# Optimization experiments

Measured on AMD Instinct MI355X. Metric: run time of the kernel, lower is better.

## Reference

```python
import jax, jax.numpy as jnp
import numpy as np

RADIUS = 5
EPS = 1e-08


def _box_blur(x, r):
    """Normalized (2r+1)x(2r+1) box filter with reflect padding, NCHW."""
    k = 2 * r + 1
    B, C, H, W = x.shape
    xp = jnp.pad(x, ((0, 0), (0, 0), (r, r), (r, r)), mode='reflect')
    y = xp.reshape(B * C, 1, H + 2 * r, W + 2 * r)
    kh = jnp.ones((1, 1, k, 1), x.dtype) / k
    kw = jnp.ones((1, 1, 1, k), x.dtype) / k
    y = jax.lax.conv_general_dilated(y, kh, (1, 1), 'VALID')
    y = jax.lax.conv_general_dilated(y, kw, (1, 1), 'VALID')
    return y.reshape(B, C, H, W)


def setup_inputs() -> dict:
    key = jax.random.key(0)
    k1, k2 = jax.random.split(key)
    feat = jax.random.uniform(k1, (8, 16, 512, 512), dtype=jnp.float32)
    img = jax.random.uniform(k2, (8, 1, 512, 512), dtype=jnp.float32)
    return {"feat": feat, "img": img}


def reference(feat, img):
    r, eps = RADIUS, EPS
    # scalar-guidance guided filter (guidance img has 1 channel)
    mean_I = _box_blur(img, r)                  # [B,1,H,W]
    mean_p = _box_blur(feat, r)                 # [B,D,H,W]
    corr_I = _box_blur(img * img, r)            # [B,1,H,W]
    corr_Ip = _box_blur(img * feat, r)          # [B,D,H,W]
    var_I = corr_I - mean_I * mean_I
    cov_Ip = corr_Ip - mean_I * mean_p
    a = cov_Ip / (var_I + eps)                  # [B,D,H,W]
    b = mean_p - a * mean_I                     # [B,D,H,W]
    mean_a = _box_blur(a, r)
    mean_b = _box_blur(b, r)
    return mean_a * img + mean_b
```

## Files before the change

kernel.cpp:

```cpp
#include <hip/hip_runtime.h>

#define HH 512
#define WW 512
#define HW (512*512)
#define NB 8
#define ND 16
#define TW 64
#define TH 64
#define VR 74
#define PTW 172

__device__ __forceinline__ int reflect(int v) {
    if (v < 0) v = -v;
    if (v >= HH) v = 2*HH - 2 - v;
    return v;
}

__global__ __launch_bounds__(256) void img_stats(const float* __restrict__ img,
                                                 float2* __restrict__ miv) {
    const int VRs = 42, PTs = 86, THs = 32, TWs = 64;
    __shared__ __align__(16) float hBuf[2*VRs*PTs + 20];
    float* hF = hBuf;
    float* hP = hBuf + VRs*PTs + 20;

    int blk  = blockIdx.x;
    int tile = blk & 127;
    int b    = blk >> 7;
    int ty0  = (tile >> 3) * THs;
    int tx0  = (tile & 7)  * TWs;

    const float inv121 = 1.0f/121.0f;
    const float* ib = img + (size_t)b*HW;
    const int t = threadIdx.x;

    if (t < 252) {
        int seg = t / 84, col = t - seg*84;
        int gx = reflect(tx0 - 10 + col);
        const float* icol = ib + gx;
        int vr0 = seg*14;
        float rv[11], rq[11];
        float sv = 0.f, sq = 0.f;
        #pragma unroll
        for (int j = 0; j < 10; ++j) {
            int gy = reflect(ty0 - 10 + vr0 + j);
            float v = icol[gy*WW], q = v*v;
            rv[j] = v; rq[j] = q; sv += v; sq += q;
        }
        #pragma unroll
        for (int k = 0; k < 14; ++k) {
            int vr = vr0 + k;
            int gy = reflect(ty0 + vr);
            float v = icol[gy*WW], q = v*v;
            sv += v; sq += q;
            hF[vr*PTs + col] = sv;
            hP[vr*PTs + col] = sq;
            sv -= rv[k%11]; sq -= rq[k%11];
            rv[(k+10)%11] = v; rq[(k+10)%11] = q;
        }
    }
    __syncthreads();

    if (t < 168) {
        int arr = t & 1;
        int j2  = t >> 1;
        int seg = (j2 >= 42) ? 1 : 0;
        int vr  = j2 - seg*42;
        int xb = seg ? 38 : 0;
        int nout = seg ? 18 : 19;
        float* rA = (arr ? hP : hF) + vr*PTs;
        float2 ring[5];
        float T = 0.f;
        #pragma unroll
        for (int j = 0; j < 5; ++j) {
            float2 v = *(float2*)(rA + xb + 2*j);
            ring[j] = v; T += v.x + v.y;
        }
        #pragma unroll
        for (int k2 = 0; k2 < 19; ++k2) {
            if (k2 < nout) {
                int hc = xb + 2*k2;
                float2 p = *(float2*)(rA + hc + 10);
                float2 q = ring[k2 % 5];
                float O0 = T + p.x;
                float O1 = O0 + p.y - q.x;
                T = O1 - q.y;
                ring[k2 % 5] = p;
                float2 o; o.x = O0*inv121; o.y = O1*inv121;
                *(float2*)(rA + hc + 10*seg) = o;
            }
        }
    }
    __syncthreads();

    float2* mb = miv + (size_t)b*HW;
    for (int i = t; i < THs*TWs; i += 256) {
        int y = i >> 6, x = i & 63;
        int vr = y + 5, hc = x + 5;
        int slot = hc + ((hc >= 38) ? 10 : 0);
        float mI  = hF[vr*PTs + slot];
        float mII = hP[vr*PTs + slot];
        float var = mII - mI*mI;
        float2 o; o.x = mI; o.y = 1.0f / (var + 1e-8f);
        mb[(ty0 + y)*WW + tx0 + x] = o;
    }
}

__global__ __launch_bounds__(512) void guided_main(const float* __restrict__ feat,
                                                   const float* __restrict__ img,
                                                   const float2* __restrict__ miv,
                                                   float* __restrict__ out) {
    __shared__ __align__(16) float S[VR*PTW];

    int blk  = blockIdx.x;
    int tile = blk & 63;
    int bd   = blk >> 6;
    int b    = bd >> 4;
    int ty0  = (tile >> 3) * TH;
    int tx0  = (tile & 7)  * TW;

    const float inv121 = 1.0f/121.0f;
    const float* fb   = feat + (size_t)bd*HW;
    const float* ib   = img  + (size_t)b*HW;
    const float2* mivb = miv + (size_t)b*HW;
    const int t = threadIdx.x;

    if (t < 504) {
        int seg = t / 84, col = t - seg*84;
        int gx = reflect(tx0 - 10 + col);
        const float* fcol = fb + gx;
        const float* icol = ib + gx;
        int vr0 = seg*13;
        float rf[11], rp[11];
        float sf = 0.f, sp = 0.f;
        #pragma unroll
        for (int j = 0; j < 10; ++j) {
            int gy = reflect(ty0 - 10 + vr0 + j);
            float f = fcol[gy*WW], im = icol[gy*WW];
            float p = f*im;
            rf[j] = f; rp[j] = p; sf += f; sp += p;
        }
        #pragma unroll
        for (int k = 0; k < 13; ++k) {
            int vr = vr0 + k;
            if (vr < VR) {
                int gy = reflect(ty0 + vr);
                float f = fcol[gy*WW], im = icol[gy*WW];
                float p = f*im;
                sf += f; sp += p;
                float2 st; st.x = sf; st.y = sp;
                *(float2*)(S + vr*PTW + 2*col) = st;
                sf -= rf[k%11]; sp -= rp[k%11];
                rf[(k+10)%11] = f; rp[(k+10)%11] = p;
            }
        }
    }
    __syncthreads();

    if (t < 148) {
        int seg = (t >= 74) ? 1 : 0;
        int vr  = t - seg*74;
        float* row = S + vr*PTW;
        int xbu = seg*19;
        int nout = seg ? 18 : 19;
        float4 ring[5];
        float TF = 0.f, TP = 0.f;
        #pragma unroll
        for (int j = 0; j < 5; ++j) {
            float4 v = *(float4*)(row + 4*(xbu + j));
            ring[j] = v; TF += v.x + v.z; TP += v.y + v.w;
        }
        float4 pre[2];
        #pragma unroll
        for (int j = 0; j < 2; ++j)
            pre[j] = *(float4*)(row + 4*(xbu + 5 + j));
        #pragma unroll
        for (int k = 0; k < 19; ++k) {
            if (k < nout) {
                float4 p = pre[k & 1];
                int nk = k + 2;
                if (nk < nout) pre[k & 1] = *(float4*)(row + 4*(xbu + 5 + nk));
                float4 q = ring[k % 5];
                float O0f = TF + p.x;
                float O1f = O0f + p.z - q.x;
                TF = O1f - q.z;
                float O0p = TP + p.y;
                float O1p = O0p + p.w - q.y;
                TP = O1p - q.w;
                ring[k % 5] = p;
                float4 o;
                o.x = O0f*inv121; o.y = O0p*inv121;
                o.z = O1f*inv121; o.w = O1p*inv121;
                *(float4*)(row + 4*(k + xbu + 5*seg)) = o;
            }
        }
    }
    __syncthreads();

    {
        const int NJ = VR*37;
        int i = t;
        float* cell = S;
        float4 mc = {};
        float2 g0 = {}, g1 = {};
        if (i < NJ) {
            int y = i / 37, u = i - y*37;
            int su = u + ((u >= 19) ? 5 : 0);
            cell = S + y*PTW + 4*su;
            mc = *(float4*)cell;
            int gy = reflect(ty0 - 5 + y);
            const float2* mrow = mivb + gy*WW;
            int gx0 = tx0 - 5 + 2*u;
            g0 = mrow[reflect(gx0)];
            g1 = mrow[reflect(gx0+1)];
        }
        while (i < NJ) {
            int inext = i + 512;
            float* celln = cell;
            float4 mcn = {};
            float2 g0n = {}, g1n = {};
            if (inext < NJ) {
                int yn = inext / 37, un = inext - yn*37;
                int sun = un + ((un >= 19) ? 5 : 0);
                celln = S + yn*PTW + 4*sun;
                mcn = *(float4*)celln;
                int gyn = reflect(ty0 - 5 + yn);
                const float2* mrown = mivb + gyn*WW;
                int gx0n = tx0 - 5 + 2*un;
                g0n = mrown[reflect(gx0n)];
                g1n = mrown[reflect(gx0n+1)];
            }
            float a0 = (mc.y - g0.x*mc.x) * g0.y;
            float b0 = mc.x - a0*g0.x;
            float a1 = (mc.w - g1.x*mc.z) * g1.y;
            float b1 = mc.z - a1*g1.x;
            float4 o; o.x = a0; o.y = b0; o.z = a1; o.w = b1;
            *(float4*)cell = o;
            i = inext; cell = celln; mc = mcn; g0 = g0n; g1 = g1n;
        }
    }
    __syncthreads();

    if (t < 148) {
        int seg = (t >= 74) ? 1 : 0;
        int c   = t - seg*74;
        int sw  = 2*(c + ((c >= 38) ? 10 : 0));
        int y0  = seg*32;
        float2 ring[11];
        float sa = 0.f, sb = 0.f;
        #pragma unroll
        for (int j = 0; j < 10; ++j) {
            float2 v = *(float2*)(S + (y0+j)*PTW + sw);
            ring[j] = v; sa += v.x; sb += v.y;
        }
        float2 pre[2];
        #pragma unroll
        for (int j = 0; j < 2; ++j)
            pre[j] = *(float2*)(S + (y0+10+j)*PTW + sw);
        #pragma unroll
        for (int k = 0; k < 32; ++k) {
            float2 v = pre[k & 1];
            if (k + 2 < 32) pre[k & 1] = *(float2*)(S + (y0+12+k)*PTW + sw);
            sa += v.x; sb += v.y;
            int wrow = y0 + k + 10*seg;
            float2 o; o.x = sa; o.y = sb;
            *(float2*)(S + wrow*PTW + sw) = o;
            sa -= ring[k%11].x; sb -= ring[k%11].y;
            ring[(k+10)%11] = v;
        }
    }
    __syncthreads();

    if (t < 128) {
        int seg = t >> 6, row = t & 63;
        int prow = row + ((row >= 32) ? 10 : 0);
        float* rw = S + prow*PTW;
        int ub = seg*16;
        float4 ring[5];
        float TA = 0.f, TB = 0.f;
        #pragma unroll
        for (int j = 0; j < 5; ++j) {
            int u = ub + j; int su = u + ((u >= 19) ? 5 : 0);
            float4 v = *(float4*)(rw + 4*su);
            ring[j] = v; TA += v.x + v.z; TB += v.y + v.w;
        }
        float4 pre[2];
        #pragma unroll
        for (int j = 0; j < 2; ++j) {
            int u = ub + 5 + j; int su = u + ((u >= 19) ? 5 : 0);
            pre[j] = *(float4*)(rw + 4*su);
        }
        #pragma unroll
        for (int k = 0; k < 16; ++k) {
            float4 p = pre[k & 1];
            if (k + 2 < 16) {
                int u = ub + 7 + k; int su = u + ((u >= 19) ? 5 : 0);
                pre[k & 1] = *(float4*)(rw + 4*su);
            }
            float4 q = ring[k % 5];
            float A0 = TA + p.x;
            float A1 = A0 + p.z - q.x;
            TA = A1 - q.z;
            float B0 = TB + p.y;
            float B1 = B0 + p.w - q.y;
            TB = B1 - q.w;
            ring[k % 5] = p;
            float4 o; o.x = A0; o.y = B0; o.z = A1; o.w = B1;
            *(float4*)(rw + 4*(ub + k) + 40*seg) = o;
        }
    }
    __syncthreads();

    float* ob = out + (size_t)bd*HW;
    for (int i = t; i < TH*32; i += 512) {
        int row = i >> 5, u = i & 31;
        int prow = row + ((row >= 32) ? 10 : 0);
        int ww = 4*u + ((u >= 16) ? 40 : 0);
        float4 s4 = *(float4*)(S + prow*PTW + ww);
        int gy = ty0 + row;
        int x0 = 2*u;
        float2 im2 = *(const float2*)(ib + gy*WW + tx0 + x0);
        float2 o;
        o.x = (s4.x*im2.x + s4.y)*inv121;
        o.y = (s4.z*im2.y + s4.w)*inv121;
        *(float2*)(ob + gy*WW + tx0 + x0) = o;
    }
}

extern "C" void kernel_launch(void* const* d_in, const int* in_sizes, int n_in,
                              void* d_out, int out_size, void* d_ws, size_t ws_size,
                              hipStream_t stream) {
    const float* feat = (const float*)d_in[0];
    const float* img  = (const float*)d_in[1];
    float* out  = (float*)d_out;
    float2* miv = (float2*)d_ws;

    img_stats<<<NB*128, 256, 0, stream>>>(img, miv);
    guided_main<<<NB*ND*64, 512, 0, stream>>>(feat, img, miv, out);
}
```

Measured before the change: 146.5 us.

## Fuse horizontal box pass with output epilogue across 256 threads

The final horizontal sliding-window pass now runs on 256 threads, each covering 8 column pairs instead of 16, and writes the output directly from registers. The shared-memory write-back, the extra barrier and the separate output loop are removed. Guidance-image values are loaded as float4 up front and results are stored as float4 runs. This doubles parallelism in that stage and drops one LDS round trip and a sync, at the cost of more redundant window warm-up loads per thread.

Measured after the change: 158.8 us. +8.4%, slower.

```diff
diff --git a/kernel.cpp b/kernel.cpp
--- a/kernel.cpp
+++ b/kernel.cpp
@@ -270,32 +270,30 @@
     }
     __syncthreads();
 
-    if (t < 128) {
+    if (t < 256) {
         int seg = t >> 6, row = t & 63;
         int prow = row + ((row >= 32) ? 10 : 0);
-        float* rw = S + prow*PTW;
-        int ub = seg*16;
+        const float* rw = S + prow*PTW;
+        int ub = 8*seg;
+        int gy = ty0 + row;
+        const float* irow = ib + gy*WW + tx0 + 2*ub;
+        float4 img4[4];
+        #pragma unroll
+        for (int j = 0; j < 4; ++j)
+            img4[j] = *(const float4*)(irow + 4*j);
         float4 ring[5];
         float TA = 0.f, TB = 0.f;
         #pragma unroll
         for (int j = 0; j < 5; ++j) {
             int u = ub + j; int su = u + ((u >= 19) ? 5 : 0);
-            float4 v = *(float4*)(rw + 4*su);
+            float4 v = *(const float4*)(rw + 4*su);
             ring[j] = v; TA += v.x + v.z; TB += v.y + v.w;
         }
-        float4 pre[2];
-        #pragma unroll
-        for (int j = 0; j < 2; ++j) {
-            int u = ub + 5 + j; int su = u + ((u >= 19) ? 5 : 0);
-            pre[j] = *(float4*)(rw + 4*su);
-        }
-        #pragma unroll
-        for (int k = 0; k < 16; ++k) {
-            float4 p = pre[k & 1];
-            if (k + 2 < 16) {
-                int u = ub + 7 + k; int su = u + ((u >= 19) ? 5 : 0);
-                pre[k & 1] = *(float4*)(rw + 4*su);
-            }
+        float4 ov[4];
+        #pragma unroll
+        for (int k = 0; k < 8; ++k) {
+            int u = ub + 5 + k; int su = u + ((u >= 19) ? 5 : 0);
+            float4 p = *(const float4*)(rw + 4*su);
             float4 q = ring[k % 5];
             float A0 = TA + p.x;
             float A1 = A0 + p.z - q.x;
@@ -304,25 +302,17 @@
             float B1 = B0 + p.w - q.y;
             TB = B1 - q.w;
             ring[k % 5] = p;
-            float4 o; o.x = A0; o.y = B0; o.z = A1; o.w = B1;
-            *(float4*)(rw + 4*(ub + k) + 40*seg) = o;
-        }
-    }
-    __syncthreads();
-
-    float* ob = out + (size_t)bd*HW;
-    for (int i = t; i < TH*32; i += 512) {
-        int row = i >> 5, u = i & 31;
-        int prow = row + ((row >= 32) ? 10 : 0);
-        int ww = 4*u + ((u >= 16) ? 40 : 0);
-        float4 s4 = *(float4*)(S + prow*PTW + ww);
-        int gy = ty0 + row;
-        int x0 = 2*u;
-        float2 im2 = *(const float2*)(ib + gy*WW + tx0 + x0);
-        float2 o;
-        o.x = (s4.x*im2.x + s4.y)*inv121;
-        o.y = (s4.z*im2.y + s4.w)*inv121;
-        *(float2*)(ob + gy*WW + tx0 + x0) = o;
+            float i0 = (k & 1) ? img4[k>>1].z : img4[k>>1].x;
+            float i1 = (k & 1) ? img4[k>>1].w : img4[k>>1].y;
+            float o0 = (A0*i0 + B0)*inv121;
+            float o1 = (A1*i1 + B1)*inv121;
+            if (k & 1) { ov[k>>1].z = o0; ov[k>>1].w = o1; }
+            else       { ov[k>>1].x = o0; ov[k>>1].y = o1; }
+        }
+        float* orow = out + (size_t)bd*HW + gy*WW + tx0 + 2*ub;
+        #pragma unroll
+        for (int j = 0; j < 4; ++j)
+            *(float4*)(orow + 4*j) = ov[j];
     }
 }
 
```

## Process two feature channels per block with half-height tiles

Applied to the files above, without the earlier changes.

Each block now handles two feature channels over a 32x64 tile instead of one channel over a 64x64 tile. Image and guidance-stat loads and the index math are shared across both channels, and each thread carries two independent accumulation chains for more ILP. The cost is a larger vertical halo relative to useful output (42 rows loaded for 32 produced), about the same shared memory per block, and more registers per thread. Fewer threads are active in each stage, which could reduce latency hiding.

After: 164.4 us. +12.3%, slower.

```diff
diff --git a/kernel.cpp b/kernel.cpp
--- a/kernel.cpp
+++ b/kernel.cpp
@@ -6,8 +6,8 @@
 #define NB 8
 #define ND 16
 #define TW 64
-#define TH 64
-#define VR 74
+#define TH 32
+#define VR 42
 #define PTW 172
 
 __device__ __forceinline__ int reflect(int v) {
@@ -109,88 +109,118 @@
                                                    const float* __restrict__ img,
                                                    const float2* __restrict__ miv,
                                                    float* __restrict__ out) {
-    __shared__ __align__(16) float S[VR*PTW];
+    __shared__ __align__(16) float S[2*VR*PTW];
+    float* S0 = S;
+    float* S1 = S + VR*PTW;
 
     int blk  = blockIdx.x;
-    int tile = blk & 63;
-    int bd   = blk >> 6;
-    int b    = bd >> 4;
+    int tile = blk & 127;
+    int cp   = blk >> 7;
+    int b    = cp >> 3;
+    int bd0  = b*ND + (cp & 7)*2;
     int ty0  = (tile >> 3) * TH;
     int tx0  = (tile & 7)  * TW;
 
     const float inv121 = 1.0f/121.0f;
-    const float* fb   = feat + (size_t)bd*HW;
+    const float* fb0  = feat + (size_t)bd0*HW;
+    const float* fb1  = fb0 + HW;
     const float* ib   = img  + (size_t)b*HW;
     const float2* mivb = miv + (size_t)b*HW;
     const int t = threadIdx.x;
 
-    if (t < 504) {
+    if (t < 252) {
         int seg = t / 84, col = t - seg*84;
         int gx = reflect(tx0 - 10 + col);
-        const float* fcol = fb + gx;
-        const float* icol = ib + gx;
-        int vr0 = seg*13;
-        float rf[11], rp[11];
-        float sf = 0.f, sp = 0.f;
+        const float* f0c = fb0 + gx;
+        const float* f1c = fb1 + gx;
+        const float* ic  = ib + gx;
+        int vr0 = seg*14;
+        float rf0[11], rp0[11], rf1[11], rp1[11];
+        float sf0=0.f, sp0=0.f, sf1=0.f, sp1=0.f;
         #pragma unroll
         for (int j = 0; j < 10; ++j) {
             int gy = reflect(ty0 - 10 + vr0 + j);
-            float f = fcol[gy*WW], im = icol[gy*WW];
-            float p = f*im;
-            rf[j] = f; rp[j] = p; sf += f; sp += p;
-        }
-        #pragma unroll
-        for (int k = 0; k < 13; ++k) {
+            float im = ic[gy*WW];
+            float f0 = f0c[gy*WW], f1 = f1c[gy*WW];
+            float p0 = f0*im, p1 = f1*im;
+            rf0[j]=f0; rp0[j]=p0; rf1[j]=f1; rp1[j]=p1;
+            sf0+=f0; sp0+=p0; sf1+=f1; sp1+=p1;
+        }
+        #pragma unroll
+        for (int k = 0; k < 14; ++k) {
             int vr = vr0 + k;
-            if (vr < VR) {
-                int gy = reflect(ty0 + vr);
-                float f = fcol[gy*WW], im = icol[gy*WW];
-                float p = f*im;
-                sf += f; sp += p;
-                float2 st; st.x = sf; st.y = sp;
-                *(float2*)(S + vr*PTW + 2*col) = st;
-                sf -= rf[k%11]; sp -= rp[k%11];
-                rf[(k+10)%11] = f; rp[(k+10)%11] = p;
-            }
-        }
-    }
-    __syncthreads();
-
-    if (t < 148) {
-        int seg = (t >= 74) ? 1 : 0;
-        int vr  = t - seg*74;
-        float* row = S + vr*PTW;
+            int gy = reflect(ty0 + vr);
+            float im = ic[gy*WW];
+            float f0 = f0c[gy*WW], f1 = f1c[gy*WW];
+            float p0 = f0*im, p1 = f1*im;
+            sf0+=f0; sp0+=p0; sf1+=f1; sp1+=p1;
+            float2 s0v; s0v.x=sf0; s0v.y=sp0;
+            float2 s1v; s1v.x=sf1; s1v.y=sp1;
+            *(float2*)(S0 + vr*PTW + 2*col) = s0v;
+            *(float2*)(S1 + vr*PTW + 2*col) = s1v;
+            sf0-=rf0[k%11]; sp0-=rp0[k%11]; sf1-=rf1[k%11]; sp1-=rp1[k%11];
+            rf0[(k+10)%11]=f0; rp0[(k+10)%11]=p0;
+            rf1[(k+10)%11]=f1; rp1[(k+10)%11]=p1;
+        }
+    }
+    __syncthreads();
+
+    if (t < 84) {
+        int seg = (t >= 42) ? 1 : 0;
+        int vr  = t - seg*42;
+        float* r0 = S0 + vr*PTW;
+        float* r1 = S1 + vr*PTW;
         int xbu = seg*19;
         int nout = seg ? 18 : 19;
-        float4 ring[5];
-        float TF = 0.f, TP = 0.f;
+        float4 rg0[5], rg1[5];
+        float TF0=0.f, TP0=0.f, TF1=0.f, TP1=0.f;
         #pragma unroll
         for (int j = 0; j < 5; ++j) {
-            float4 v = *(float4*)(row + 4*(xbu + j));
-            ring[j] = v; TF += v.x + v.z; TP += v.y + v.w;
-        }
-        float4 pre[2];
-        #pragma unroll
-        for (int j = 0; j < 2; ++j)
-            pre[j] = *(float4*)(row + 4*(xbu + 5 + j));
+            float4 v0 = *(float4*)(r0 + 4*(xbu + j));
+            float4 v1 = *(float4*)(r1 + 4*(xbu + j));
+            rg0[j] = v0; TF0 += v0.x + v0.z; TP0 += v0.y + v0.w;
+            rg1[j] = v1; TF1 += v1.x + v1.z; TP1 += v1.y + v1.w;
+        }
+        float4 pr0[2], pr1[2];
+        #pragma unroll
+        for (int j = 0; j < 2; ++j) {
+            pr0[j] = *(float4*)(r0 + 4*(xbu + 5 + j));
+            pr1[j] = *(float4*)(r1 + 4*(xbu + 5 + j));
+        }
         #pragma unroll
         for (int k = 0; k < 19; ++k) {
             if (k < nout) {
-                float4 p = pre[k & 1];
+                float4 p0 = pr0[k & 1];
+                float4 p1 = pr1[k & 1];
                 int nk = k + 2;
-                if (nk < nout) pre[k & 1] = *(float4*)(row + 4*(xbu + 5 + nk));
-                float4 q = ring[k % 5];
-                float O0f = TF + p.x;
-                float O1f = O0f + p.z - q.x;
-                TF = O1f - q.z;
-                float O0p = TP + p.y;
-                float O1p = O0p + p.w - q.y;
-                TP = O1p - q.w;
-                ring[k % 5] = p;
-                float4 o;
-                o.x = O0f*inv121; o.y = O0p*inv121;
-                o.z = O1f*inv121; o.w = O1p*inv121;
-                *(float4*)(row + 4*(k + xbu + 5*seg)) = o;
+                if (nk < nout) {
+                    pr0[k & 1] = *(float4*)(r0 + 4*(xbu + 5 + nk));
+                    pr1[k & 1] = *(float4*)(r1 + 4*(xbu + 5 + nk));
+                }
+                float4 q0 = rg0[k % 5];
+                float4 q1 = rg1[k % 5];
+                float O0f = TF0 + p0.x;
+                float O1f = O0f + p0.z - q0.x;
+                TF0 = O1f - q0.z;
+                float O0p = TP0 + p0.y;
+                float O1p = O0p + p0.w - q0.y;
+                TP0 = O1p - q0.w;
+                rg0[k % 5] = p0;
+                float4 o0;
+                o0.x = O0f*inv121; o0.y = O0p*inv121;
+                o0.z = O1f*inv121; o0.w = O1p*inv121;
+                *(float4*)(r0 + 4*(k + xbu + 5*seg)) = o0;
+                float G0f = TF1 + p1.x;
+                float G1f = G0f + p1.z - q1.x;
+                TF1 = G1f - q1.z;
+                float G0p = TP1 + p1.y;
+                float G1p = G0p + p1.w - q1.y;
+                TP1 = G1p - q1.w;
+                rg1[k % 5] = p1;
+                float4 o1;
+                o1.x = G0f*inv121; o1.y = G0p*inv121;
+                o1.z = G1f*inv121; o1.w = G1p*inv121;
+                *(float4*)(r1 + 4*(k + xbu + 5*seg)) = o1;
             }
         }
     }
@@ -199,14 +229,16 @@
     {
         const int NJ = VR*37;
         int i = t;
-        float* cell = S;
-        float4 mc = {};
+        float *c0 = S0, *c1 = S1;
+        float4 m0 = {}, m1 = {};
         float2 g0 = {}, g1 = {};
         if (i < NJ) {
             int y = i / 37, u = i - y*37;
             int su = u + ((u >= 19) ? 5 : 0);
-            cell = S + y*PTW + 4*su;
-            mc = *(float4*)cell;
+            c0 = S0 + y*PTW + 4*su;
+            c1 = S1 + y*PTW + 4*su;
+            m0 = *(float4*)c0;
+            m1 = *(float4*)c1;
             int gy = reflect(ty0 - 5 + y);
             const float2* mrow = mivb + gy*WW;
             int gx0 = tx0 - 5 + 2*u;
@@ -215,27 +247,39 @@
         }
         while (i < NJ) {
             int inext = i + 512;
-            float* celln = cell;
-            float4 mcn = {};
+            float *c0n = c0, *c1n = c1;
+            float4 m0n = {}, m1n = {};
             float2 g0n = {}, g1n = {};
             if (inext < NJ) {
                 int yn = inext / 37, un = inext - yn*37;
                 int sun = un + ((un >= 19) ? 5 : 0);
-                celln = S + yn*PTW + 4*sun;
-                mcn = *(float4*)celln;
+                c0n = S0 + yn*PTW + 4*sun;
+                c1n = S1 + yn*PTW + 4*sun;
+                m0n = *(float4*)c0n;
+                m1n = *(float4*)c1n;
                 int gyn = reflect(ty0 - 5 + yn);
                 const float2* mrown = mivb + gyn*WW;
                 int gx0n = tx0 - 5 + 2*un;
                 g0n = mrown[reflect(gx0n)];
                 g1n = mrown[reflect(gx0n+1)];
             }
-            float a0 = (mc.y - g0.x*mc.x) * g0.y;
-            float b0 = mc.x - a0*g0.x;
-            float a1 = (mc.w - g1.x*mc.z) * g1.y;
-            float b1 = mc.z - a1*g1.x;
-            float4 o; o.x = a0; o.y = b0; o.z = a1; o.w = b1;
-            *(float4*)cell = o;
-            i = inext; cell = celln; mc = mcn; g0 = g0n; g1 = g1n;
+            {
+                float a0 = (m0.y - g0.x*m0.x) * g0.y;
+                float b0 = m0.x - a0*g0.x;
+                float a1 = (m0.w - g1.x*m0.z) * g1.y;
+                float b1 = m0.z - a1*g1.x;
+                float4 o; o.x = a0; o.y = b0; o.z = a1; o.w = b1;
+                *(float4*)c0 = o;
+            }
+            {
+                float a0 = (m1.y - g0.x*m1.x) * g0.y;
+                float b0 = m1.x - a0*g0.x;
+                float a1 = (m1.w - g1.x*m1.z) * g1.y;
+                float b1 = m1.z - a1*g1.x;
+                float4 o; o.x = a0; o.y = b0; o.z = a1; o.w = b1;
+                *(float4*)c1 = o;
+            }
+            i = inext; c0 = c0n; c1 = c1n; m0 = m0n; m1 = m1n; g0 = g0n; g1 = g1n;
         }
     }
     __syncthreads();
@@ -244,85 +288,117 @@
         int seg = (t >= 74) ? 1 : 0;
         int c   = t - seg*74;
         int sw  = 2*(c + ((c >= 38) ? 10 : 0));
-        int y0  = seg*32;
-        float2 ring[11];
-        float sa = 0.f, sb = 0.f;
+        int y0  = seg*16;
+        float2 r0[11], r1[11];
+        float sa0=0.f, sb0=0.f, sa1=0.f, sb1=0.f;
         #pragma unroll
         for (int j = 0; j < 10; ++j) {
-            float2 v = *(float2*)(S + (y0+j)*PTW + sw);
-            ring[j] = v; sa += v.x; sb += v.y;
-        }
-        float2 pre[2];
-        #pragma unroll
-        for (int j = 0; j < 2; ++j)
-            pre[j] = *(float2*)(S + (y0+10+j)*PTW + sw);
-        #pragma unroll
-        for (int k = 0; k < 32; ++k) {
-            float2 v = pre[k & 1];
-            if (k + 2 < 32) pre[k & 1] = *(float2*)(S + (y0+12+k)*PTW + sw);
-            sa += v.x; sb += v.y;
+            float2 v0 = *(float2*)(S0 + (y0+j)*PTW + sw);
+            float2 v1 = *(float2*)(S1 + (y0+j)*PTW + sw);
+            r0[j] = v0; sa0 += v0.x; sb0 += v0.y;
+            r1[j] = v1; sa1 += v1.x; sb1 += v1.y;
+        }
+        float2 p0[2], p1[2];
+        #pragma unroll
+        for (int j = 0; j < 2; ++j) {
+            p0[j] = *(float2*)(S0 + (y0+10+j)*PTW + sw);
+            p1[j] = *(float2*)(S1 + (y0+10+j)*PTW + sw);
+        }
+        #pragma unroll
+        for (int k = 0; k < 16; ++k) {
+            float2 v0 = p0[k & 1];
+            float2 v1 = p1[k & 1];
+            if (k + 2 < 16) {
+                p0[k & 1] = *(float2*)(S0 + (y0+12+k)*PTW + sw);
+                p1[k & 1] = *(float2*)(S1 + (y0+12+k)*PTW + sw);
+            }
+            sa0 += v0.x; sb0 += v0.y;
+            sa1 += v1.x; sb1 += v1.y;
             int wrow = y0 + k + 10*seg;
-            float2 o; o.x = sa; o.y = sb;
-            *(float2*)(S + wrow*PTW + sw) = o;
-            sa -= ring[k%11].x; sb -= ring[k%11].y;
-            ring[(k+10)%11] = v;
-        }
-    }
-    __syncthreads();
-
-    if (t < 128) {
-        int seg = t >> 6, row = t & 63;
-        int prow = row + ((row >= 32) ? 10 : 0);
-        float* rw = S + prow*PTW;
+            float2 o0; o0.x = sa0; o0.y = sb0;
+            float2 o1; o1.x = sa1; o1.y = sb1;
+            *(float2*)(S0 + wrow*PTW + sw) = o0;
+            *(float2*)(S1 + wrow*PTW + sw) = o1;
+            sa0 -= r0[k%11].x; sb0 -= r0[k%11].y;
+            sa1 -= r1[k%11].x; sb1 -= r1[k%11].y;
+            r0[(k+10)%11] = v0;
+            r1[(k+10)%11] = v1;
+        }
+    }
+    __syncthreads();
+
+    if (t < 64) {
+        int seg = t >> 5, row = t & 31;
+        int prow = row + ((row >= 16) ? 10 : 0);
+        float* w0 = S0 + prow*PTW;
+        float* w1 = S1 + prow*PTW;
         int ub = seg*16;
-        float4 ring[5];
-        float TA = 0.f, TB = 0.f;
+        float4 rg0[5], rg1[5];
+        float TA0=0.f, TB0=0.f, TA1=0.f, TB1=0.f;
         #pragma unroll
         for (int j = 0; j < 5; ++j) {
             int u = ub + j; int su = u + ((u >= 19) ? 5 : 0);
-            float4 v = *(float4*)(rw + 4*su);
-            ring[j] = v; TA += v.x + v.z; TB += v.y + v.w;
-        }
-        float4 pre[2];
+            float4 v0 = *(float4*)(w0 + 4*su);
+            float4 v1 = *(float4*)(w1 + 4*su);
+            rg0[j] = v0; TA0 += v0.x + v0.z; TB0 += v0.y + v0.w;
+            rg1[j] = v1; TA1 += v1.x + v1.z; TB1 += v1.y + v1.w;
+        }
+        float4 pr0[2], pr1[2];
         #pragma unroll
         for (int j = 0; j < 2; ++j) {
             int u = ub + 5 + j; int su = u + ((u >= 19) ? 5 : 0);
-            pre[j] = *(float4*)(rw + 4*su);
+            pr0[j] = *(float4*)(w0 + 4*su);
+            pr1[j] = *(float4*)(w1 + 4*su);
         }
         #pragma unroll
         for (int k = 0; k < 16; ++k) {
-            float4 p = pre[k & 1];
+            float4 p0 = pr0[k & 1];
+            float4 p1 = pr1[k & 1];
             if (k + 2 < 16) {
                 int u = ub + 7 + k; int su = u + ((u >= 19) ? 5 : 0);
-                pre[k & 1] = *(float4*)(rw + 4*su);
-            }
-            float4 q = ring[k % 5];
-            float A0 = TA + p.x;
-            float A1 = A0 + p.z - q.x;
-            TA = A1 - q.z;
-            float B0 = TB + p.y;
-            float B1 = B0 + p.w - q.y;
-            TB = B1 - q.w;
-            ring[k % 5] = p;
-            float4 o; o.x = A0; o.y = B0; o.z = A1; o.w = B1;
-            *(float4*)(rw + 4*(ub + k) + 40*seg) = o;
-        }
-    }
-    __syncthreads();
-
-    float* ob = out + (size_t)bd*HW;
-    for (int i = t; i < TH*32; i += 512) {
-        int row = i >> 5, u = i & 31;
-        int prow = row + ((row >= 32) ? 10 : 0);
+                pr0[k & 1] = *(float4*)(w0 + 4*su);
+                pr1[k & 1] = *(float4*)(w1 + 4*su);
+            }
+            float4 q0 = rg0[k % 5];
+            float4 q1 = rg1[k % 5];
+            float A0 = TA0 + p0.x;
+            float A1 = A0 + p0.z - q0.x;
+            TA0 = A1 - q0.z;
+            float B0 = TB0 + p0.y;
+            float B1 = B0 + p0.w - q0.y;
+            TB0 = B1 - q0.w;
+            rg0[k % 5] = p0;
+            float4 o0; o0.x = A0; o0.y = B0; o0.z = A1; o0.w = B1;
+            *(float4*)(w0 + 4*(ub + k) + 40*seg) = o0;
+            float C0 = TA1 + p1.x;
+            float C1 = C0 + p1.z - q1.x;
+            TA1 = C1 - q1.z;
+            float D0 = TB1 + p1.y;
+            float D1 = D0 + p1.w - q1.y;
+            TB1 = D1 - q1.w;
+            rg1[k % 5] = p1;
+            float4 o1; o1.x = C0; o1.y = D0; o1.z = C1; o1.w = D1;
+            *(float4*)(w1 + 4*(ub + k) + 40*seg) = o1;
+        }
+    }
+    __syncthreads();
+
+    float* ob0 = out + (size_t)bd0*HW;
+    float* ob1 = ob0 + HW;
+    for (int i = t; i < 2*TH*32; i += 512) {
+        int u = i & 31, row = (i >> 5) & 31, ch = i >> 10;
+        const float* Sx = ch ? S1 : S0;
+        float* ox = ch ? ob1 : ob0;
+        int prow = row + ((row >= 16) ? 10 : 0);
         int ww = 4*u + ((u >= 16) ? 40 : 0);
-        float4 s4 = *(float4*)(S + prow*PTW + ww);
+        float4 s4 = *(const float4*)(Sx + prow*PTW + ww);
         int gy = ty0 + row;
         int x0 = 2*u;
         float2 im2 = *(const float2*)(ib + gy*WW + tx0 + x0);
         float2 o;
         o.x = (s4.x*im2.x + s4.y)*inv121;
         o.y = (s4.z*im2.y + s4.w)*inv121;
-        *(float2*)(ob + gy*WW + tx0 + x0) = o;
+        *(float2*)(ox + gy*WW + tx0 + x0) = o;
     }
 }
 
@@ -335,5 +411,5 @@
     float2* miv = (float2*)d_ws;
 
     img_stats<<<NB*128, 256, 0, stream>>>(img, miv);
-    guided_main<<<NB*ND*64, 512, 0, stream>>>(feat, img, miv, out);
+    guided_main<<<NB*(ND/2)*128, 512, 0, stream>>>(feat, img, miv, out);
 }
```
